# Optimization experiments

Measured on AMD Instinct MI355X. Metric: run time of the kernel, lower is better.

## Reference

```python
import jax, jax.numpy as jnp
import numpy as np

N_NODES = 50000
N_EDGES = 800000
NUM_GRAPHS = 256
H = 128          # h_dim
C = H + 1        # CGConv channels = 129
Z = 2 * C + 1    # concat(x_i, x_j, edge_attr) = 259
N_GRAPH_LAYERS = 5
N_FC = 3
OUT_DIM = 1


def setup_inputs() -> dict:
    key = jax.random.key(0)
    ks = jax.random.split(key, 12)
    atoms = jax.random.randint(ks[0], (N_NODES,), 0, 119)
    pos = jax.random.normal(ks[1], (N_NODES, 3), dtype=jnp.float32)
    edge_index = jax.random.randint(ks[2], (2, N_EDGES), 0, N_NODES)
    batch = jnp.sort(jax.random.randint(ks[3], (N_NODES,), 0, NUM_GRAPHS))
    s = 0.05
    emb = jax.random.normal(ks[4], (119, H), dtype=jnp.float32)
    Wf = jax.random.normal(ks[5], (N_GRAPH_LAYERS, Z, C), dtype=jnp.float32) * s
    bf = jnp.zeros((N_GRAPH_LAYERS, C), dtype=jnp.float32)
    Ws = jax.random.normal(ks[6], (N_GRAPH_LAYERS, Z, C), dtype=jnp.float32) * s
    bs = jnp.zeros((N_GRAPH_LAYERS, C), dtype=jnp.float32)
    Wfc = jax.random.normal(ks[7], (N_FC, C, C), dtype=jnp.float32) * s
    bfc = jnp.zeros((N_FC, C), dtype=jnp.float32)
    Wout = jax.random.normal(ks[8], (C, OUT_DIM), dtype=jnp.float32) * s
    bout = jnp.zeros((OUT_DIM,), dtype=jnp.float32)
    return {"atoms": atoms, "pos": pos, "edge_index": edge_index, "batch": batch,
            "emb": emb, "Wf": Wf, "bf": bf, "Ws": Ws, "bs": bs,
            "Wfc": Wfc, "bfc": bfc, "Wout": Wout, "bout": bout}


def reference(atoms, pos, edge_index, batch, emb, Wf, bf, Ws, bs, Wfc, bfc, Wout, bout):
    n = atoms.shape[0]
    src, dst = edge_index[0], edge_index[1]  # PyG: x_j = x[src], x_i = x[dst], aggregate at dst
    # edge_attr = ||pos[src] - pos[dst]||, shape [E, 1]
    edge_attr = jnp.linalg.norm(pos[src] - pos[dst], axis=-1, keepdims=True)
    # node features: atom embedding + z-coordinate -> [N, 129]
    x = jnp.concatenate([emb[atoms], pos[:, 2:3]], axis=-1)
    for l in range(Wf.shape[0]):
        z = jnp.concatenate([x[dst], x[src], edge_attr], axis=-1)  # [E, 259]
        m = jax.nn.sigmoid(z @ Wf[l] + bf[l]) * jax.nn.softplus(z @ Ws[l] + bs[l])
        x = x + jax.ops.segment_sum(m, dst, num_segments=n)  # CGConv: aggr='add' + residual
    # mean pooling per graph
    sums = jax.ops.segment_sum(x, batch, num_segments=NUM_GRAPHS)
    cnts = jax.ops.segment_sum(jnp.ones((n, 1), x.dtype), batch, num_segments=NUM_GRAPHS)
    g = sums / jnp.maximum(cnts, 1.0)
    for l in range(Wfc.shape[0]):
        g = g @ Wfc[l] + bfc[l]
    return g @ Wout + bout
```

## Files before the change

### kernel.cpp

```cpp
#include <hip/hip_runtime.h>
#include <math.h>

#define N_NODES 50000
#define N_EDGES 800000
#define NUM_GRAPHS 256
#define NPADROWS 50048
#define CAP 64
#define XR 128
#define XSG 132
#define SCLN -1.44269504088896f
#define SCLP 1.44269504088896f
#define C693 0.69314718056f
#define LROW 264

typedef __attribute__((ext_vector_type(8))) short short8;
typedef __attribute__((ext_vector_type(4))) float f32x4;
typedef __attribute__((ext_vector_type(2))) float f32x2;

__device__ __forceinline__ float fast_rcp(float x) {
#if __has_builtin(__builtin_amdgcn_rcpf)
  return __builtin_amdgcn_rcpf(x);
#else
  return 1.0f / x;
#endif
}
__device__ __forceinline__ float EX2(float x) {
#if __has_builtin(__builtin_amdgcn_exp2f)
  return __builtin_amdgcn_exp2f(x);
#else
  return exp2f(x);
#endif
}
__device__ __forceinline__ float LG2(float x) {
#if __has_builtin(__builtin_amdgcn_logf)
  return __builtin_amdgcn_logf(x);
#else
  return log2f(x);
#endif
}
__device__ __forceinline__ unsigned f2bf(float x) {
  unsigned u = __float_as_uint(x);
  return (u + 0x7fffu + ((u >> 16) & 1u)) >> 16;
}
__device__ __forceinline__ float u2f(unsigned u) { return __uint_as_float(u); }
__device__ __forceinline__ f32x2 mk2(float a, float b) {
  f32x2 r; r.x = a; r.y = b; return r;
}
__device__ __forceinline__ f32x2 unp(unsigned u) {
  return mk2(u2f(u << 16), u2f(u & 0xffff0000u));
}
__device__ __forceinline__ void edge_ch2(f32x2 gf, f32x2 gs, float cmul, f32x2& acc) {
  f32x2 den = mk2(EX2(gf.x), EX2(gf.y)) + 1.0f;
  f32x2 lg = mk2(LG2(1.0f + EX2(-fabsf(gs.x))), LG2(1.0f + EX2(-fabsf(gs.y))));
  f32x2 sp = lg + __builtin_elementwise_max(gs, (f32x2)0.0f);
  f32x2 rt = mk2(fast_rcp(den.x), fast_rcp(den.y)) * sp;
  acc = __builtin_elementwise_fma(rt, (f32x2)cmul, acc);
}

__global__ void init_x(const int* __restrict__ atoms, const float* __restrict__ pos,
                       const float* __restrict__ emb, float* __restrict__ xf,
                       float* __restrict__ x128c, unsigned* __restrict__ xbu,
                       float4* __restrict__ pos4) {
  int n = blockIdx.x;
  int t = threadIdx.x;
  int a = atoms[n];
  float2 e = *(const float2*)(emb + (size_t)a * 128 + 2 * t);
  xf[(size_t)n * XR + 2 * t] = e.x;
  xf[(size_t)n * XR + 2 * t + 1] = e.y;
  xbu[(size_t)n * 64 + t] = f2bf(e.x) | (f2bf(e.y) << 16);
  if (t == 0) x128c[n] = pos[n * 3 + 2];
  if (t == 1) pos4[n] = make_float4(pos[3 * n], pos[3 * n + 1], pos[3 * n + 2], 0.f);
}

__global__ void prep_b(const float* __restrict__ Wf, const float* __restrict__ Ws,
                       uint4* __restrict__ Bp, float* __restrict__ W128) {
  int idx = blockIdx.x * 256 + threadIdx.x;
  if (idx < 5 * 4 * 9 * 4 * 64) {
    int lane = idx & 63;
    int t = idx >> 6;
    int ks = t & 3; t >>= 2;
    int ct = t % 9; t /= 9;
    int g = t & 3;
    int l = t >> 2;
    const float* W = (g >= 2) ? Ws : Wf;
    int col = ct * 16 + (lane & 15);
    int kb = ks * 32 + (lane >> 4) * 8;
    unsigned u[4];
#pragma unroll
    for (int p = 0; p < 4; ++p) {
      unsigned lo = 0, hi = 0;
      if (col < 129) {
        int k0 = kb + 2 * p, k1 = k0 + 1;
        int r0 = (g & 1) ? 129 + k0 : k0;
        int r1 = (g & 1) ? 129 + k1 : k1;
        lo = f2bf(W[(size_t)(l * 259 + r0) * 129 + col]);
        hi = f2bf(W[(size_t)(l * 259 + r1) * 129 + col]);
      }
      u[p] = lo | (hi << 16);
    }
    Bp[idx] = make_uint4(u[0], u[1], u[2], u[3]);
  } else {
    int j = idx - 5 * 4 * 9 * 4 * 64;
    if (j >= 5 * 4 * 129) return;
    int c = j % 129;
    int t = j / 129;
    int g = t & 3;
    int l = t >> 2;
    const float* W = (g >= 2) ? Ws : Wf;
    int row = (g & 1) ? 257 : 128;
    W128[(l * 4 + g) * 129 + c] = W[(size_t)(l * 259 + row) * 129 + c];
  }
}

__global__ void build_csr(const int* __restrict__ ei, const float4* __restrict__ pos4,
                          int* __restrict__ cnt, int2* __restrict__ csr) {
  int e = blockIdx.x * 256 + threadIdx.x;
  if (e >= N_EDGES) return;
  int s = ei[e];
  int d = ei[N_EDGES + e];
  float4 ps = pos4[s];
  float4 pd = pos4[d];
  float dx = ps.x - pd.x, dy = ps.y - pd.y, dz = ps.z - pd.z;
  float ea = sqrtf(dx * dx + dy * dy + dz * dz);
  int p = atomicAdd(&cnt[d], 1);
  if (p < CAP) csr[d * CAP + p] = make_int2(s, __float_as_int(ea));
}

__global__ void offsets_k(const int* __restrict__ batch, int* __restrict__ goff) {
  int n = blockIdx.x * 256 + threadIdx.x;
  if (n > N_NODES) return;
  int b = (n < N_NODES) ? batch[n] : NUM_GRAPHS;
  int bp = (n > 0) ? batch[n - 1] : -1;
  for (int g = bp + 1; g <= b; ++g) goff[g] = n;
}

__global__ __launch_bounds__(256) void gemm_mfma(
    const unsigned* __restrict__ xbu, const float* __restrict__ x128c,
    const uint4* __restrict__ Bp, const float* __restrict__ W128,
    const float* __restrict__ bfL, const float* __restrict__ bsL,
    unsigned short* __restrict__ Pdh, unsigned short* __restrict__ Pfs,
    unsigned* __restrict__ Pd128c, unsigned* __restrict__ Pc128, int layer) {
  __shared__ short smA[32 * 136];
  __shared__ unsigned short ldsD[32 * LROW];
  __shared__ unsigned short ldsS[32 * LROW];
  int n0 = blockIdx.x * 32;
  int tid = threadIdx.x;
  for (int ch = tid; ch < 512; ch += 256) {
    int row = ch >> 4, cq = ch & 15;
    *(uint4*)(&smA[row * 136 + cq * 8]) =
        *(const uint4*)(xbu + (size_t)(n0 + row) * 64 + cq * 4);
  }
  __syncthreads();
  int g = tid >> 6;
  int l = tid & 63;
  int q = l >> 4, c16 = l & 15;
  const short8* Bp8 = (const short8*)Bp;
  int bbase = (layer * 4 + g) * 9 * 4;
  f32x4 acc[2][9];
#pragma unroll
  for (int rt = 0; rt < 2; ++rt)
#pragma unroll
    for (int ct = 0; ct < 9; ++ct) acc[rt][ct] = (f32x4){0.f, 0.f, 0.f, 0.f};
#pragma unroll
  for (int ks = 0; ks < 4; ++ks) {
    short8 a0 = *(const short8*)(&smA[c16 * 136 + (ks * 4 + q) * 8]);
    short8 a1 = *(const short8*)(&smA[(16 + c16) * 136 + (ks * 4 + q) * 8]);
#pragma unroll
    for (int ct = 0; ct < 9; ++ct) {
      short8 b = Bp8[(size_t)(bbase + ct * 4 + ks) * 64 + l];
      acc[0][ct] = __builtin_amdgcn_mfma_f32_16x16x32_bf16(a0, b, acc[0][ct], 0, 0, 0);
      acc[1][ct] = __builtin_amdgcn_mfma_f32_16x16x32_bf16(a1, b, acc[1][ct], 0, 0, 0);
    }
  }
  const float* W1g = W128 + (layer * 4 + g) * 129;
  float x128[2][4];
#pragma unroll
  for (int rt = 0; rt < 2; ++rt)
#pragma unroll
    for (int r = 0; r < 4; ++r)
      x128[rt][r] = x128c[n0 + rt * 16 + q * 4 + r];
  float scale = (g < 2) ? SCLN : SCLP;
  unsigned short* ldsO = (g & 1) ? ldsS : ldsD;
  int soff = (g >= 2) ? 2 : 0;
  unsigned short* c128p = (g & 1) ? (unsigned short*)Pc128 : (unsigned short*)Pd128c;
  int c128o = (g >= 2) ? 1 : 0;
#pragma unroll
  for (int ct = 0; ct < 9; ++ct) {
    int col = ct * 16 + c16;
    float w1 = (col <= 128) ? W1g[col] : 0.0f;
    float bias = 0.0f;
    if (g == 0 && col <= 128) bias = bfL[col];
    if (g == 2 && col <= 128) bias = bsL[col];
#pragma unroll
    for (int rt = 0; rt < 2; ++rt) {
#pragma unroll
      for (int r = 0; r < 4; ++r) {
        int rl = rt * 16 + q * 4 + r;
        float v = scale * (acc[rt][ct][r] + x128[rt][r] * w1 + bias);
        unsigned short bv = (unsigned short)f2bf(v);
        if (col < 128) {
          ldsO[rl * LROW + ((col >> 1) << 2) + soff + (col & 1)] = bv;
        } else if (col == 128) {
          c128p[2 * (size_t)(n0 + rl) + c128o] = bv;
        }
      }
    }
  }
  __syncthreads();
#pragma unroll
  for (int i = tid; i < 2048; i += 256) {
    int img = i >> 10;
    int c = i & 1023;
    int row = c >> 5, part = c & 31;
    const unsigned short* src = (img ? ldsS : ldsD) + row * LROW + part * 8;
    unsigned short* dst = (img ? Pfs : Pdh) + (size_t)(n0 + row) * 256 + part * 8;
    *(uint4*)dst = *(const uint4*)src;
  }
}

__global__ __launch_bounds__(256) void edge_agg(
    const unsigned short* __restrict__ Pdh, const unsigned short* __restrict__ Pfs,
    const unsigned* __restrict__ Pd128c, const unsigned* __restrict__ Pc128,
    float* __restrict__ xf, float* __restrict__ x128c, unsigned* __restrict__ xbu,
    const int* __restrict__ cnt, const int2* __restrict__ csr,
    const float* __restrict__ WfL, const float* __restrict__ WsL) {
  int lane = threadIdx.x & 63;
  int half = lane >> 5;
  int l5 = lane & 31;
  int n = blockIdx.x * 4 + (threadIdx.x >> 6);
  if (n >= N_NODES) return;
  int nu = __builtin_amdgcn_readfirstlane(n);
  const float* wfl = WfL + 258 * 129;
  const float* wsl = WsL + 258 * 129;
  uint4 pdv = *(const uint4*)(Pdh + (size_t)nu * 256 + 8 * l5);
  f32x2 bfa = unp(pdv.x), bsa = unp(pdv.y), bfb = unp(pdv.z), bsb = unp(pdv.w);
  float2 wfa0 = *(const float2*)(wfl + 4 * l5);
  float2 wfb0 = *(const float2*)(wfl + 4 * l5 + 2);
  float2 wsa0 = *(const float2*)(wsl + 4 * l5);
  float2 wsb0 = *(const float2*)(wsl + 4 * l5 + 2);
  f32x2 wfa = mk2(SCLN * wfa0.x, SCLN * wfa0.y), wfb = mk2(SCLN * wfb0.x, SCLN * wfb0.y);
  f32x2 wsa = mk2(SCLP * wsa0.x, SCLP * wsa0.y), wsb = mk2(SCLP * wsb0.x, SCLP * wsb0.y);
  unsigned pd1 = Pd128c[nu];
  float bfc8 = u2f(pd1 << 16), bsc8 = u2f(pd1 & 0xffff0000u);
  float wfc8 = SCLN * wfl[128], wsc8 = SCLP * wsl[128];
  int m = cnt[nu];
  if (m > CAP) m = CAP;
  const int2* cbh = csr + (size_t)nu * CAP + half;
  const uint4* Pfq = (const uint4*)Pfs;
  float maskC = half ? 0.0f : C693;
  f32x2 accA = (f32x2)0.0f, accB = (f32x2)0.0f;

#define COMPUTE(se, gg, CM)                                                    \
  {                                                                            \
    f32x2 ea_ = (f32x2)__int_as_float(se.y);                                   \
    edge_ch2(__builtin_elementwise_fma(ea_, wfa, bfa + unp(gg.x)),             \
             __builtin_elementwise_fma(ea_, wsa, bsa + unp(gg.y)), CM, accA);  \
    edge_ch2(__builtin_elementwise_fma(ea_, wfb, bfb + unp(gg.z)),             \
             __builtin_elementwise_fma(ea_, wsb, bsb + unp(gg.w)), CM, accB);  \
  }

  int Pf = m >> 1;
  int2 sc = make_int2(0, 0);
  uint4 gc = make_uint4(0, 0, 0, 0);
  if (Pf > 0) {
    sc = cbh[0];
    gc = Pfq[(size_t)sc.x * 32 + l5];
  }
  for (int p = 0; p < Pf; ++p) {
    int2 sn = sc;
    uint4 gn = gc;
    if (p + 1 < Pf) {
      sn = cbh[2 * (p + 1)];
      gn = Pfq[(size_t)sn.x * 32 + l5];
    }
    COMPUTE(sc, gc, C693);
    sc = sn;
    gc = gn;
  }
  if (m & 1) {
    int2 qt = csr[(size_t)nu * CAP + m - 1];
    uint4 gt = Pfq[(size_t)qt.x * 32 + l5];
    COMPUTE(qt, gt, maskC);
  }
#undef COMPUTE

  accA.x += __shfl_xor(accA.x, 32, 64);
  accA.y += __shfl_xor(accA.y, 32, 64);
  accB.x += __shfl_xor(accB.x, 32, 64);
  accB.y += __shfl_xor(accB.y, 32, 64);

  float v2 = 0.f;
  if (lane < m) {
    int2 se = csr[(size_t)nu * CAP + lane];
    float ea = __int_as_float(se.y);
    unsigned pc = Pc128[se.x];
    float f2 = u2f(pc << 16), s2 = u2f(pc & 0xffff0000u);
    float gf2 = fmaf(ea, wfc8, bfc8 + f2);
    float gs2 = fmaf(ea, wsc8, bsc8 + s2);
    float sp2 = LG2(1.0f + EX2(-fabsf(gs2))) + fmaxf(gs2, 0.0f);
    v2 = C693 * fast_rcp(1.0f + EX2(gf2)) * sp2;
  }
#pragma unroll
  for (int off = 32; off; off >>= 1) v2 += __shfl_down(v2, off, 64);

  size_t xo = (size_t)nu * XR;
  if (half == 0) {
    float4 xv = *(const float4*)(xf + xo + 4 * l5);
    float4 res = make_float4(xv.x + accA.x, xv.y + accA.y, xv.z + accB.x, xv.w + accB.y);
    *(float4*)(xf + xo + 4 * l5) = res;
    *(uint2*)(xbu + (size_t)nu * 64 + 2 * l5) =
        make_uint2(f2bf(res.x) | (f2bf(res.y) << 16), f2bf(res.z) | (f2bf(res.w) << 16));
  }
  if (lane == 0) x128c[nu] += v2;
}

__global__ void pool2(const float* __restrict__ xf, const float* __restrict__ x128c,
                      const int* __restrict__ goff, float* __restrict__ gsum) {
  int gph = blockIdx.x >> 2;
  int q = blockIdx.x & 3;
  int t = threadIdx.x;
  if (t >= 129) return;
  int s = goff[gph], e = goff[gph + 1];
  int len = e - s;
  int chunk = (len + 3) >> 2;
  int a = s + q * chunk;
  int b = a + chunk; if (b > e) b = e;
  if (a >= b) return;
  float acc = 0.f;
  if (t < 128) {
    for (int n = a; n < b; ++n) acc += xf[(size_t)n * XR + t];
  } else {
    for (int n = a; n < b; ++n) acc += x128c[n];
  }
  atomicAdd(&gsum[gph * XSG + t], acc);
}

__global__ void fcout(const float* __restrict__ gsum, const int* __restrict__ goff,
                      const float* __restrict__ Wfc, const float* __restrict__ bfc,
                      const float* __restrict__ Wout, const float* __restrict__ bout,
                      float* __restrict__ out) {
  __shared__ float buf[2][XSG];
  __shared__ float red[3];
  int i = blockIdx.x;
  int t = threadIdx.x;
  int len = goff[i + 1] - goff[i];
  float inv = fast_rcp(fmaxf((float)len, 1.0f));
  if (t < 129) buf[0][t] = gsum[i * XSG + t] * inv;
  __syncthreads();
  int cur = 0;
#pragma unroll
  for (int l = 0; l < 3; ++l) {
    float s = 0.f;
    if (t < 129) {
      s = bfc[l * 129 + t];
      const float* W = Wfc + (size_t)l * 129 * 129;
#pragma unroll 4
      for (int k = 0; k < 129; ++k) s += buf[cur][k] * W[k * 129 + t];
    }
    __syncthreads();
    if (t < 129) buf[1 - cur][t] = s;
    cur = 1 - cur;
    __syncthreads();
  }
  float p = (t < 129) ? buf[cur][t] * Wout[t] : 0.f;
#pragma unroll
  for (int off = 32; off; off >>= 1) p += __shfl_down(p, off, 64);
  if ((t & 63) == 0) red[t >> 6] = p;
  __syncthreads();
  if (t == 0) out[i] = red[0] + red[1] + red[2] + bout[0];
}

extern "C" void kernel_launch(void* const* d_in, const int* in_sizes, int n_in,
                              void* d_out, int out_size, void* d_ws, size_t ws_size,
                              hipStream_t stream) {
  const int* atoms = (const int*)d_in[0];
  const float* pos = (const float*)d_in[1];
  const int* ei = (const int*)d_in[2];
  const int* batch = (const int*)d_in[3];
  const float* emb = (const float*)d_in[4];
  const float* Wf = (const float*)d_in[5];
  const float* bfp = (const float*)d_in[6];
  const float* Ws = (const float*)d_in[7];
  const float* bsp = (const float*)d_in[8];
  const float* Wfc = (const float*)d_in[9];
  const float* bfc = (const float*)d_in[10];
  const float* Wout = (const float*)d_in[11];
  const float* bout = (const float*)d_in[12];
  float* outp = (float*)d_out;

  uint4* Bp = (uint4*)d_ws;
  float* xf = (float*)(Bp + 46080);
  float* x128c = xf + (size_t)NPADROWS * XR;
  unsigned* xbu = (unsigned*)(x128c + NPADROWS);
  unsigned short* Pdh = (unsigned short*)(xbu + (size_t)NPADROWS * 64);
  unsigned short* Pfs = Pdh + (size_t)NPADROWS * 256;
  float4* pos4 = (float4*)(Pfs + (size_t)NPADROWS * 256);
  float* W128 = (float*)(pos4 + N_NODES);
  float* gsum = W128 + 2580;
  int* goff = (int*)(gsum + 256 * XSG);
  int* cnt = goff + 260;
  int2* csr = (int2*)(cnt + N_NODES + 2);
  unsigned* Pd128c = (unsigned*)(csr + (size_t)N_NODES * CAP);
  unsigned* Pc128 = Pd128c + NPADROWS;

  hipMemsetAsync(cnt, 0, N_NODES * sizeof(int), stream);
  hipMemsetAsync(gsum, 0, 256 * XSG * sizeof(float), stream);

  init_x<<<N_NODES, 64, 0, stream>>>(atoms, pos, emb, xf, x128c, xbu, pos4);
  prep_b<<<(5 * 4 * 9 * 4 * 64 + 5 * 4 * 129 + 255) / 256, 256, 0, stream>>>(Wf, Ws, Bp,
                                                                             W128);
  build_csr<<<(N_EDGES + 255) / 256, 256, 0, stream>>>(ei, pos4, cnt, csr);
  offsets_k<<<(N_NODES + 256) / 256, 256, 0, stream>>>(batch, goff);

  for (int l = 0; l < 5; ++l) {
    gemm_mfma<<<NPADROWS / 32, 256, 0, stream>>>(xbu, x128c, Bp, W128, bfp + l * 129,
                                                 bsp + l * 129, Pdh, Pfs, Pd128c,
                                                 Pc128, l);
    edge_agg<<<(N_NODES + 3) / 4, 256, 0, stream>>>(Pdh, Pfs, Pd128c, Pc128, xf, x128c,
                                                    xbu, cnt, csr,
                                                    Wf + (size_t)l * 259 * 129,
                                                    Ws + (size_t)l * 259 * 129);
  }

  pool2<<<NUM_GRAPHS * 4, 192, 0, stream>>>(xf, x128c, goff, gsum);
  fcout<<<NUM_GRAPHS, 192, 0, stream>>>(gsum, goff, Wfc, bfc, Wout, bout, outp);
}
```

Baseline: 757.2 us.

## Replace transcendental intrinsics with packed polynomial exp2/log/rcp and widen CSR loads

```diff
diff --git a/kernel.cpp b/kernel.cpp
--- a/kernel.cpp
+++ b/kernel.cpp
@@ -38,6 +38,13 @@
   return log2f(x);
 #endif
 }
+__device__ __forceinline__ float LDX(float x, int k) {
+#if __has_builtin(__builtin_amdgcn_ldexpf)
+  return __builtin_amdgcn_ldexpf(x, k);
+#else
+  return ldexpf(x, k);
+#endif
+}
 __device__ __forceinline__ unsigned f2bf(float x) {
   unsigned u = __float_as_uint(x);
   return (u + 0x7fffu + ((u >> 16) & 1u)) >> 16;
@@ -49,11 +56,49 @@
 __device__ __forceinline__ f32x2 unp(unsigned u) {
   return mk2(u2f(u << 16), u2f(u & 0xffff0000u));
 }
+
+__device__ __forceinline__ f32x2 pexp2(f32x2 x) {
+  const f32x2 MAG = (f32x2)12582912.0f;
+  f32x2 xm = x + MAG;
+  f32x2 f = x - (xm - MAG);
+  int kx = __float_as_int(xm.x) - 0x4B400000;
+  int ky = __float_as_int(xm.y) - 0x4B400000;
+  f32x2 p = (f32x2)0.0013333558f;
+  p = __builtin_elementwise_fma(p, f, (f32x2)0.0096181291f);
+  p = __builtin_elementwise_fma(p, f, (f32x2)0.0555041087f);
+  p = __builtin_elementwise_fma(p, f, (f32x2)0.2402265069f);
+  p = __builtin_elementwise_fma(p, f, (f32x2)0.6931471806f);
+  p = __builtin_elementwise_fma(p, f, (f32x2)1.0f);
+  return mk2(LDX(p.x, kx), LDX(p.y, ky));
+}
+__device__ __forceinline__ f32x2 plog21p(f32x2 u) {
+  f32x2 t = u + (f32x2)(-0.5f);
+  f32x2 p = (f32x2)(-0.0070365f);
+  p = __builtin_elementwise_fma(p, t, (f32x2)0.0120625f);
+  p = __builtin_elementwise_fma(p, t, (f32x2)(-0.0211095f));
+  p = __builtin_elementwise_fma(p, t, (f32x2)0.0379969f);
+  p = __builtin_elementwise_fma(p, t, (f32x2)(-0.0712442f));
+  p = __builtin_elementwise_fma(p, t, (f32x2)0.1424884f);
+  p = __builtin_elementwise_fma(p, t, (f32x2)(-0.3205989f));
+  p = __builtin_elementwise_fma(p, t, (f32x2)0.9617967f);
+  p = __builtin_elementwise_fma(p, t, (f32x2)0.5849625f);
+  return p;
+}
+__device__ __forceinline__ f32x2 prcp(f32x2 d) {
+  f32x2 r = mk2(__int_as_float(0x7EF311C3 - __float_as_int(d.x)),
+                __int_as_float(0x7EF311C3 - __float_as_int(d.y)));
+  f32x2 e = __builtin_elementwise_fma(-d, r, (f32x2)1.0f);
+  r = __builtin_elementwise_fma(r, e, r);
+  e = __builtin_elementwise_fma(-d, r, (f32x2)1.0f);
+  r = __builtin_elementwise_fma(r, e, r);
+  return r;
+}
 __device__ __forceinline__ void edge_ch2(f32x2 gf, f32x2 gs, float cmul, f32x2& acc) {
-  f32x2 den = mk2(EX2(gf.x), EX2(gf.y)) + 1.0f;
-  f32x2 lg = mk2(LG2(1.0f + EX2(-fabsf(gs.x))), LG2(1.0f + EX2(-fabsf(gs.y))));
-  f32x2 sp = lg + __builtin_elementwise_max(gs, (f32x2)0.0f);
-  f32x2 rt = mk2(fast_rcp(den.x), fast_rcp(den.y)) * sp;
+  gf = __builtin_elementwise_min(gf, (f32x2)126.0f);
+  f32x2 den = pexp2(gf) + 1.0f;
+  f32x2 u = pexp2(-__builtin_elementwise_abs(gs));
+  f32x2 sp = plog21p(u) + __builtin_elementwise_max(gs, (f32x2)0.0f);
+  f32x2 rt = prcp(den) * sp;
   acc = __builtin_elementwise_fma(rt, (f32x2)cmul, acc);
 }
 
@@ -245,14 +290,15 @@
   float wfc8 = SCLN * wfl[128], wsc8 = SCLP * wsl[128];
   int m = cnt[nu];
   if (m > CAP) m = CAP;
-  const int2* cbh = csr + (size_t)nu * CAP + half;
+  const int4* cb4 = (const int4*)(csr + (size_t)nu * CAP);
   const uint4* Pfq = (const uint4*)Pfs;
   float maskC = half ? 0.0f : C693;
   f32x2 accA = (f32x2)0.0f, accB = (f32x2)0.0f;
 
-#define COMPUTE(se, gg, CM)                                                    \
+#define GATHER(qq) Pfq[(size_t)(half ? qq.z : qq.x) * 32 + l5]
+#define COMPUTE(qq, gg, CM)                                                    \
   {                                                                            \
-    f32x2 ea_ = (f32x2)__int_as_float(se.y);                                   \
+    f32x2 ea_ = (f32x2)__int_as_float(half ? qq.w : qq.y);                     \
     edge_ch2(__builtin_elementwise_fma(ea_, wfa, bfa + unp(gg.x)),             \
              __builtin_elementwise_fma(ea_, wsa, bsa + unp(gg.y)), CM, accA);  \
     edge_ch2(__builtin_elementwise_fma(ea_, wfb, bfb + unp(gg.z)),             \
@@ -260,28 +306,33 @@
   }
 
   int Pf = m >> 1;
-  int2 sc = make_int2(0, 0);
+  int4 qc = make_int4(0, 0, 0, 0);
   uint4 gc = make_uint4(0, 0, 0, 0);
   if (Pf > 0) {
-    sc = cbh[0];
-    gc = Pfq[(size_t)sc.x * 32 + l5];
+    qc = cb4[0];
+    gc = GATHER(qc);
   }
   for (int p = 0; p < Pf; ++p) {
-    int2 sn = sc;
+    int4 qn = qc;
     uint4 gn = gc;
     if (p + 1 < Pf) {
-      sn = cbh[2 * (p + 1)];
-      gn = Pfq[(size_t)sn.x * 32 + l5];
+      qn = cb4[p + 1];
+      gn = GATHER(qn);
     }
-    COMPUTE(sc, gc, C693);
-    sc = sn;
+    COMPUTE(qc, gc, C693);
+    qc = qn;
     gc = gn;
   }
   if (m & 1) {
-    int2 qt = csr[(size_t)nu * CAP + m - 1];
+    int4 qt = cb4[Pf];
+    f32x2 ea_ = (f32x2)__int_as_float(qt.y);
     uint4 gt = Pfq[(size_t)qt.x * 32 + l5];
-    COMPUTE(qt, gt, maskC);
-  }
+    edge_ch2(__builtin_elementwise_fma(ea_, wfa, bfa + unp(gt.x)),
+             __builtin_elementwise_fma(ea_, wsa, bsa + unp(gt.y)), maskC, accA);
+    edge_ch2(__builtin_elementwise_fma(ea_, wfb, bfb + unp(gt.z)),
+             __builtin_elementwise_fma(ea_, wsb, bsb + unp(gt.w)), maskC, accB);
+  }
+#undef GATHER
 #undef COMPUTE
 
   accA.x += __shfl_xor(accA.x, 32, 64);
```

Result: slower. 931.2 us (+23.0%).
